# Performance work log

Measured on AMD Instinct MI355X. Metric: run time of the kernel, lower is better.

Reference implementation:

```python
import jax, jax.numpy as jnp
import numpy as np

N_NODES = 100000


def _gcn_conv(x, W, b, src, dst, n):
    """torch_geometric GCNConv: add self-loops, sym-normalize, x@W, scatter-add."""
    x = x @ W                                   # [n, out]
    loop = jnp.arange(n, dtype=src.dtype)
    src_f = jnp.concatenate([src, loop])        # [E+n]
    dst_f = jnp.concatenate([dst, loop])
    deg = jax.ops.segment_sum(jnp.ones_like(dst_f, dtype=x.dtype), dst_f,
                              num_segments=n)   # in-degree incl. self-loop
    dinv = jnp.where(deg > 0, jax.lax.rsqrt(deg), 0.0)
    norm = dinv[src_f] * dinv[dst_f]            # [E+n]
    msg = x[src_f] * norm[:, None]              # [E+n, out]
    out = jax.ops.segment_sum(msg, dst_f, num_segments=n)
    return out + b


def setup_inputs() -> dict:
    key = jax.random.key(0)
    k1, k2, k3, k4 = jax.random.split(key, 4)
    ninp = 64
    E = 1600000
    edge_index = jax.random.randint(k1, (2, E), 0, N_NODES, dtype=jnp.int64)
    emb = jax.random.normal(k2, (N_NODES, ninp), dtype=jnp.float32) * (1.0 / np.sqrt(ninp))
    W1 = jax.random.normal(k3, (ninp, 2 * ninp), dtype=jnp.float32) * (1.0 / np.sqrt(ninp))
    b1 = jnp.zeros((2 * ninp,), dtype=jnp.float32)
    W2 = jax.random.normal(k4, (2 * ninp, ninp), dtype=jnp.float32) * (1.0 / np.sqrt(2 * ninp))
    b2 = jnp.zeros((ninp,), dtype=jnp.float32)
    return {"edge_index": edge_index, "emb": emb, "W1": W1, "b1": b1, "W2": W2, "b2": b2}


def reference(edge_index, emb, W1, b1, W2, b2):
    src, dst = edge_index[0], edge_index[1]
    h = jax.nn.relu(_gcn_conv(emb, W1, b1, src, dst, N_NODES))
    # dropout: eval mode (identity)
    out = _gcn_conv(h, W2, b2, src, dst, N_NODES)
    return out
```

## Files before the change

kernel.cpp:

```cpp
#include <hip/hip_runtime.h>
#include <cstdint>
#include <cstddef>

#define N_NODES_C 100000
#define NF 64
#define BW 512
#define NB 196
#define CHUNK 8192
#define SORT_CAP 9216

static inline size_t align256(size_t x) { return (x + 255) & ~size_t(255); }

typedef __attribute__((ext_vector_type(8))) short bf16x8;
typedef __attribute__((ext_vector_type(4))) float f32x4;

__device__ inline float bf2f(unsigned short u) { return __uint_as_float(((unsigned)u) << 16); }
__device__ inline unsigned short f2bf(float x) {
    unsigned u = __float_as_uint(x);
    return (unsigned short)((u + 0x7fffu + ((u >> 16) & 1u)) >> 16);
}

__global__ __launch_bounds__(1024) void bucket_count(const int* __restrict__ dst, int E,
                                                     int* __restrict__ counts) {
    __shared__ int hist[NB];
    int t = threadIdx.x;
    for (int i = t; i < NB; i += 1024) hist[i] = 0;
    __syncthreads();
    int e0 = blockIdx.x * CHUNK;
    int e1 = min(e0 + CHUNK, E);
    for (int e = e0 + t; e < e1; e += 1024) atomicAdd(&hist[dst[e] >> 9], 1);
    __syncthreads();
    for (int i = t; i < NB; i += 1024)
        if (hist[i]) atomicAdd(&counts[i], hist[i]);
}

__global__ void scan196(const int* __restrict__ counts, int* __restrict__ base196,
                        int* __restrict__ bucket_cursor, int* __restrict__ row_start, int n) {
    int lane = threadIdx.x;
    int base = 0;
    for (int c = 0; c < NB; c += 64) {
        int idx = c + lane;
        int v = (idx < NB) ? counts[idx] : 0;
        int x = v;
        #pragma unroll
        for (int d = 1; d < 64; d <<= 1) {
            int y = __shfl_up(x, d, 64);
            if (lane >= d) x += y;
        }
        if (idx < NB) { base196[idx] = base + x - v; bucket_cursor[idx] = base + x - v; }
        base += __shfl(x, 63, 64);
    }
    if (lane == 0) { base196[NB] = base; row_start[n] = base; }
}

__global__ __launch_bounds__(1024) void bin_kernel(const int* __restrict__ src,
                                                   const int* __restrict__ dst, int E,
                                                   int* __restrict__ bucket_cursor,
                                                   int* __restrict__ packed) {
    __shared__ int hist[NB];
    __shared__ int lbase[NB];
    __shared__ int lcur[NB];
    __shared__ int gbase[NB];
    __shared__ int stage[CHUNK];
    __shared__ unsigned char bid[CHUNK];
    int t = threadIdx.x;
    int e0 = blockIdx.x * CHUNK;
    int e1 = min(e0 + CHUNK, E);
    for (int i = t; i < NB; i += 1024) hist[i] = 0;
    __syncthreads();
    for (int e = e0 + t; e < e1; e += 1024) atomicAdd(&hist[dst[e] >> 9], 1);
    __syncthreads();
    if (t < 64) {
        int base = 0;
        for (int c = 0; c < NB; c += 64) {
            int idx = c + t;
            int v = (idx < NB) ? hist[idx] : 0;
            int x = v;
            #pragma unroll
            for (int d = 1; d < 64; d <<= 1) {
                int y = __shfl_up(x, d, 64);
                if (t >= d) x += y;
            }
            if (idx < NB) { lbase[idx] = base + x - v; lcur[idx] = base + x - v; }
            base += __shfl(x, 63, 64);
        }
    }
    __syncthreads();
    if (t < NB) gbase[t] = atomicAdd(&bucket_cursor[t], hist[t]);
    for (int e = e0 + t; e < e1; e += 1024) {
        int d = dst[e];
        int b = d >> 9;
        int p = atomicAdd(&lcur[b], 1);
        stage[p] = (src[e] << 9) | (d & (BW - 1));
        bid[p] = (unsigned char)b;
    }
    __syncthreads();
    int cnt = e1 - e0;
    for (int i = t; i < cnt; i += 1024) {
        int b = bid[i];
        packed[gbase[b] + (i - lbase[b])] = stage[i];
    }
}

__global__ __launch_bounds__(512) void bucket_sort_deg(const int* __restrict__ base196,
                                                       const int* __restrict__ packed,
                                                       int* __restrict__ sorted_src,
                                                       int* __restrict__ row_start,
                                                       float* __restrict__ dinv, int n) {
    __shared__ int hist[BW];
    __shared__ int cur[BW];
    __shared__ int wsum[8];
    __shared__ int sorted[SORT_CAP];
    int b = blockIdx.x;
    int node0 = b * BW;
    int nn = min(BW, n - node0);
    int base = base196[b];
    int end = base196[b + 1];
    int cnt = end - base;
    int t = threadIdx.x;
    hist[t] = 0;
    __syncthreads();
    for (int i = t; i < cnt; i += 512) atomicAdd(&hist[packed[base + i] & (BW - 1)], 1);
    __syncthreads();
    int v = hist[t];
    int lane = t & 63, w = t >> 6;
    int x = v;
    #pragma unroll
    for (int d = 1; d < 64; d <<= 1) {
        int y = __shfl_up(x, d, 64);
        if (lane >= d) x += y;
    }
    if (lane == 63) wsum[w] = x;
    __syncthreads();
    int woff = 0;
    for (int i = 0; i < w; ++i) woff += wsum[i];
    int excl = woff + x - v;
    cur[t] = excl;
    if (t < nn) {
        row_start[node0 + t] = base + excl;
        dinv[node0 + t] = rsqrtf((float)(v + 1));
    }
    __syncthreads();
    for (int i = t; i < cnt; i += 512) {
        int pk = packed[base + i];
        int p = atomicAdd(&cur[pk & (BW - 1)], 1);
        sorted[p] = pk >> 9;
    }
    __syncthreads();
    for (int i = t; i < cnt; i += 512) sorted_src[base + i] = sorted[i];
}

__global__ __launch_bounds__(256) void prep_w(const float* __restrict__ W1,
                                              const float* __restrict__ W2,
                                              unsigned short* __restrict__ W1f,
                                              unsigned short* __restrict__ W2f) {
    int idx = blockIdx.x * 256 + threadIdx.x;
    int lane = (idx >> 3) & 63;
    int j = idx & 7;
    int kk = (lane >> 4) * 8 + j;
    int cb = lane & 15;
    if (idx < 8192) {
        int frag = idx >> 9;
        int ct = frag >> 1, ks = frag & 1;
        W1f[idx] = f2bf(W1[(ks * 32 + kk) * 128 + ct * 16 + cb]);
    } else {
        int i2 = idx - 8192;
        int frag = i2 >> 9;
        int ct = frag >> 2, ks = frag & 3;
        W2f[i2] = f2bf(W2[(ks * 32 + kk) * 64 + ct * 16 + cb]);
    }
}

__global__ __launch_bounds__(256) void scale_emb(const float* __restrict__ emb,
                                                 const float* __restrict__ dinv,
                                                 unsigned short* __restrict__ Xs, int nq) {
    int q = blockIdx.x * 256 + threadIdx.x;
    if (q >= nq) return;
    int node = q >> 4;
    float d = dinv[node];
    float4 v = ((const float4*)emb)[q];
    ushort4 u;
    u.x = f2bf(v.x * d); u.y = f2bf(v.y * d);
    u.z = f2bf(v.z * d); u.w = f2bf(v.w * d);
    *(ushort4*)&Xs[(size_t)q * 4] = u;
}

template<int OUTBF>
__global__ __launch_bounds__(256) void agg_bf16(const unsigned short* __restrict__ Xs,
                                                const float* __restrict__ dinv,
                                                const int* __restrict__ row_start,
                                                const int* __restrict__ sorted_src,
                                                const float* __restrict__ bias,
                                                void* __restrict__ outp, int n) {
    int lane = threadIdx.x & 63;
    int wid = threadIdx.x >> 6;
    int wave = blockIdx.x * (blockDim.x >> 6) + wid;
    int nwaves = gridDim.x * (blockDim.x >> 6);
    int e = lane >> 4;
    int c = lane & 15;
    const int ZOFF = -64;
    for (int i = wave; i < n; i += nwaves) {
        int s0 = row_start[i], s1 = row_start[i + 1];
        float di = dinv[i];
        ushort4 uself = *(const ushort4*)&Xs[(size_t)i * NF + 4 * c];
        float a0 = 0.f, a1 = 0.f, a2 = 0.f, a3 = 0.f;
        float g0 = 0.f, g1 = 0.f, g2 = 0.f, g3 = 0.f;
        for (int j = s0; j < s1; j += 16) {
            int b0 = j + 4 * e;
            int sj0 = b0, sj1 = b0 + 1, sj2 = b0 + 2, sj3 = b0 + 3;
            int i0 = sorted_src[min(sj0, s1 - 1)];
            int i1 = sorted_src[min(sj1, s1 - 1)];
            int i2 = sorted_src[min(sj2, s1 - 1)];
            int i3 = sorted_src[min(sj3, s1 - 1)];
            int o0 = (sj0 < s1) ? (i0 << 6) : ZOFF;
            int o1 = (sj1 < s1) ? (i1 << 6) : ZOFF;
            int o2 = (sj2 < s1) ? (i2 << 6) : ZOFF;
            int o3 = (sj3 < s1) ? (i3 << 6) : ZOFF;
            ushort4 u0 = *(const ushort4*)(Xs + o0 + 4 * c);
            ushort4 u1 = *(const ushort4*)(Xs + o1 + 4 * c);
            ushort4 u2 = *(const ushort4*)(Xs + o2 + 4 * c);
            ushort4 u3 = *(const ushort4*)(Xs + o3 + 4 * c);
            a0 += bf2f(u0.x); a1 += bf2f(u0.y); a2 += bf2f(u0.z); a3 += bf2f(u0.w);
            g0 += bf2f(u1.x); g1 += bf2f(u1.y); g2 += bf2f(u1.z); g3 += bf2f(u1.w);
            a0 += bf2f(u2.x); a1 += bf2f(u2.y); a2 += bf2f(u2.z); a3 += bf2f(u2.w);
            g0 += bf2f(u3.x); g1 += bf2f(u3.y); g2 += bf2f(u3.z); g3 += bf2f(u3.w);
        }
        a0 += g0; a1 += g1; a2 += g2; a3 += g3;
        a0 += __shfl_xor(a0, 16, 64); a1 += __shfl_xor(a1, 16, 64);
        a2 += __shfl_xor(a2, 16, 64); a3 += __shfl_xor(a3, 16, 64);
        a0 += __shfl_xor(a0, 32, 64); a1 += __shfl_xor(a1, 32, 64);
        a2 += __shfl_xor(a2, 32, 64); a3 += __shfl_xor(a3, 32, 64);
        if (e == 0) {
            a0 = di * (a0 + bf2f(uself.x));
            a1 = di * (a1 + bf2f(uself.y));
            a2 = di * (a2 + bf2f(uself.z));
            a3 = di * (a3 + bf2f(uself.w));
            if (bias) {
                float4 bb = *(const float4*)&bias[4 * c];
                a0 += bb.x; a1 += bb.y; a2 += bb.z; a3 += bb.w;
            }
            if constexpr (OUTBF) {
                unsigned short* out = (unsigned short*)outp;
                ushort4 o;
                o.x = f2bf(a0); o.y = f2bf(a1); o.z = f2bf(a2); o.w = f2bf(a3);
                *(ushort4*)&out[(size_t)i * NF + 4 * c] = o;
            } else {
                float* out = (float*)outp;
                float4 o; o.x = a0; o.y = a1; o.z = a2; o.w = a3;
                *(float4*)&out[(size_t)i * NF + 4 * c] = o;
            }
        }
    }
}

__global__ __launch_bounds__(256) void gemm_mfma(const unsigned short* __restrict__ Abf,
                                                 const unsigned short* __restrict__ W1f,
                                                 const float* __restrict__ b1,
                                                 const unsigned short* __restrict__ W2f,
                                                 const float* __restrict__ dinv,
                                                 unsigned short* __restrict__ Tbf, int n) {
    __shared__ unsigned short h_all[4][16 * 136];
    const int t = threadIdx.x;
    const int wid = t >> 6, lane = t & 63;
    const int m = lane & 15, kg = lane >> 4;
    const int wrow = blockIdx.x * 64 + wid * 16;
    unsigned short* h_lds = h_all[wid];

    int arow = wrow + m; if (arow >= n) arow = n - 1;
    bf16x8 a0 = *(const bf16x8*)&Abf[(size_t)arow * 64 + kg * 8];
    bf16x8 a1 = *(const bf16x8*)&Abf[(size_t)arow * 64 + 32 + kg * 8];

    #pragma unroll
    for (int ct = 0; ct < 8; ++ct) {
        f32x4 acc = {0.f, 0.f, 0.f, 0.f};
        bf16x8 w0 = *(const bf16x8*)&W1f[(ct * 2 + 0) * 512 + lane * 8];
        bf16x8 w1 = *(const bf16x8*)&W1f[(ct * 2 + 1) * 512 + lane * 8];
        acc = __builtin_amdgcn_mfma_f32_16x16x32_bf16(a0, w0, acc, 0, 0, 0);
        acc = __builtin_amdgcn_mfma_f32_16x16x32_bf16(a1, w1, acc, 0, 0, 0);
        float bb = b1[ct * 16 + m];
        #pragma unroll
        for (int r = 0; r < 4; ++r) {
            float v = fmaxf(acc[r] + bb, 0.f);
            h_lds[(kg * 4 + r) * 136 + ct * 16 + m] = f2bf(v);
        }
    }

    bf16x8 hf[4];
    #pragma unroll
    for (int ks = 0; ks < 4; ++ks)
        hf[ks] = *(const bf16x8*)&h_lds[m * 136 + ks * 32 + kg * 8];

    float dv[4];
    #pragma unroll
    for (int r = 0; r < 4; ++r) {
        int row = wrow + kg * 4 + r;
        dv[r] = (row < n) ? dinv[row] : 0.f;
    }
    #pragma unroll
    for (int ct = 0; ct < 4; ++ct) {
        f32x4 acc = {0.f, 0.f, 0.f, 0.f};
        #pragma unroll
        for (int ks = 0; ks < 4; ++ks) {
            bf16x8 w = *(const bf16x8*)&W2f[(ct * 4 + ks) * 512 + lane * 8];
            acc = __builtin_amdgcn_mfma_f32_16x16x32_bf16(hf[ks], w, acc, 0, 0, 0);
        }
        #pragma unroll
        for (int r = 0; r < 4; ++r) {
            int row = wrow + kg * 4 + r;
            if (row < n) Tbf[(size_t)row * 64 + ct * 16 + m] = f2bf(acc[r] * dv[r]);
        }
    }
}

extern "C" void kernel_launch(void* const* d_in, const int* in_sizes, int n_in,
                              void* d_out, int out_size, void* d_ws, size_t ws_size,
                              hipStream_t stream) {
    const int* edge = (const int*)d_in[0];
    const float* emb = (const float*)d_in[1];
    const float* W1  = (const float*)d_in[2];
    const float* b1  = (const float*)d_in[3];
    const float* W2  = (const float*)d_in[4];
    const float* b2  = (const float*)d_in[5];
    int E = in_sizes[0] / 2;
    const int* src = edge;
    const int* dst = edge + E;
    int n = N_NODES_C;

    char* p = (char*)d_ws;
    int*   row_start  = (int*)p;   p += align256((size_t)(n + 1) * 4);
    float* dinv       = (float*)p; p += align256((size_t)n * 4);
    int*   bcounts    = (int*)p;   p += align256(256 * 4);
    int*   base196    = (int*)p;   p += align256(256 * 4);
    int*   bucket_cur = (int*)p;   p += align256(256 * 4);
    unsigned short* W1f = (unsigned short*)p; p += align256(8192 * 2);
    unsigned short* W2f = (unsigned short*)p; p += align256(8192 * 2);
    int*   sorted_src = (int*)p;   p += align256((size_t)E * 4);
    char*  zpadA      = p;         p += 256;
    unsigned short* Abf = (unsigned short*)p; p += align256((size_t)n * NF * 2);
    char*  zpadX      = p;         p += 256;
    unsigned short* Xs  = (unsigned short*)p; p += align256((size_t)n * NF * 2);
    int* packed = (int*)Abf;

    prep_w<<<64, 256, 0, stream>>>(W1, W2, W1f, W2f);
    hipMemsetAsync(bcounts, 0, NB * 4, stream);
    hipMemsetAsync(zpadA, 0, 256, stream);
    hipMemsetAsync(zpadX, 0, 256, stream);
    int nbin = (E + CHUNK - 1) / CHUNK;
    bucket_count<<<nbin, 1024, 0, stream>>>(dst, E, bcounts);
    scan196<<<1, 64, 0, stream>>>(bcounts, base196, bucket_cur, row_start, n);
    bin_kernel<<<nbin, 1024, 0, stream>>>(src, dst, E, bucket_cur, packed);
    bucket_sort_deg<<<NB, 512, 0, stream>>>(base196, packed, sorted_src, row_start, dinv, n);

    int nq = n * 16;
    scale_emb<<<(nq + 255) / 256, 256, 0, stream>>>(emb, dinv, Xs, nq);
    agg_bf16<1><<<4096, 256, 0, stream>>>(Xs, dinv, row_start, sorted_src, nullptr, Abf, n);
    gemm_mfma<<<(n + 63) / 64, 256, 0, stream>>>(Abf, W1f, b1, W2f, dinv, Xs, n);
    agg_bf16<0><<<4096, 256, 0, stream>>>(Xs, dinv, row_start, sorted_src, b2, d_out, n);
}
```

Before: 150.6 us.

## Replace global atomic bucket cursors with per-chunk histogram scan for deterministic binning

Each chunk's bucket histogram is now stored to global memory, and a column-wise scan gives every chunk a fixed offset within each bucket. The binning kernel then reads these offsets instead of rescanning dst to rebuild the histogram and taking global atomic cursors. The three memsets are folded into the small scan kernel, which cuts launch count. In exchange it adds one scan kernel launch and extra histogram and partial-offset buffers in the workspace.

```diff
diff --git a/kernel.cpp b/kernel.cpp
--- a/kernel.cpp
+++ b/kernel.cpp
@@ -20,8 +20,8 @@
     return (unsigned short)((u + 0x7fffu + ((u >> 16) & 1u)) >> 16);
 }
 
-__global__ __launch_bounds__(1024) void bucket_count(const int* __restrict__ dst, int E,
-                                                     int* __restrict__ counts) {
+__global__ __launch_bounds__(1024) void count_hist(const int* __restrict__ dst, int E,
+                                                   int* __restrict__ chunk_hist) {
     __shared__ int hist[NB];
     int t = threadIdx.x;
     for (int i = t; i < NB; i += 1024) hist[i] = 0;
@@ -30,45 +30,71 @@
     int e1 = min(e0 + CHUNK, E);
     for (int e = e0 + t; e < e1; e += 1024) atomicAdd(&hist[dst[e] >> 9], 1);
     __syncthreads();
-    for (int i = t; i < NB; i += 1024)
-        if (hist[i]) atomicAdd(&counts[i], hist[i]);
-}
-
-__global__ void scan196(const int* __restrict__ counts, int* __restrict__ base196,
-                        int* __restrict__ bucket_cursor, int* __restrict__ row_start, int n) {
+    for (int i = t; i < NB; i += 1024) chunk_hist[blockIdx.x * NB + i] = hist[i];
+}
+
+__global__ void scan_cols(const int* __restrict__ chunk_hist, int nbin,
+                          int* __restrict__ gpart, int* __restrict__ colsum) {
+    int b = blockIdx.x;
     int lane = threadIdx.x;
+    int base = 0;
+    for (int c0 = 0; c0 < nbin; c0 += 64) {
+        int c = c0 + lane;
+        int v = (c < nbin) ? chunk_hist[c * NB + b] : 0;
+        int x = v;
+        #pragma unroll
+        for (int d = 1; d < 64; d <<= 1) {
+            int y = __shfl_up(x, d, 64);
+            if (lane >= d) x += y;
+        }
+        if (c < nbin) gpart[c * NB + b] = base + x - v;
+        base += __shfl(x, 63, 64);
+    }
+    if (lane == 0) colsum[b] = base;
+}
+
+__global__ void scan196b(const int* __restrict__ colsum, int* __restrict__ base196,
+                         int* __restrict__ row_start, int n,
+                         int* __restrict__ zpadA, int* __restrict__ zpadX) {
+    int lane = threadIdx.x;
+    zpadA[lane] = 0;
+    zpadX[lane] = 0;
     int base = 0;
     for (int c = 0; c < NB; c += 64) {
         int idx = c + lane;
-        int v = (idx < NB) ? counts[idx] : 0;
+        int v = (idx < NB) ? colsum[idx] : 0;
         int x = v;
         #pragma unroll
         for (int d = 1; d < 64; d <<= 1) {
             int y = __shfl_up(x, d, 64);
             if (lane >= d) x += y;
         }
-        if (idx < NB) { base196[idx] = base + x - v; bucket_cursor[idx] = base + x - v; }
+        if (idx < NB) base196[idx] = base + x - v;
         base += __shfl(x, 63, 64);
     }
     if (lane == 0) { base196[NB] = base; row_start[n] = base; }
 }
 
-__global__ __launch_bounds__(1024) void bin_kernel(const int* __restrict__ src,
-                                                   const int* __restrict__ dst, int E,
-                                                   int* __restrict__ bucket_cursor,
-                                                   int* __restrict__ packed) {
+__global__ __launch_bounds__(1024) void bin_kernel2(const int* __restrict__ src,
+                                                    const int* __restrict__ dst, int E,
+                                                    const int* __restrict__ chunk_hist,
+                                                    const int* __restrict__ gpart,
+                                                    const int* __restrict__ base196,
+                                                    int* __restrict__ packed) {
     __shared__ int hist[NB];
     __shared__ int lbase[NB];
     __shared__ int lcur[NB];
-    __shared__ int gbase[NB];
+    __shared__ int dbase[NB];
     __shared__ int stage[CHUNK];
     __shared__ unsigned char bid[CHUNK];
     int t = threadIdx.x;
-    int e0 = blockIdx.x * CHUNK;
+    int ch = blockIdx.x;
+    int e0 = ch * CHUNK;
     int e1 = min(e0 + CHUNK, E);
-    for (int i = t; i < NB; i += 1024) hist[i] = 0;
-    __syncthreads();
-    for (int e = e0 + t; e < e1; e += 1024) atomicAdd(&hist[dst[e] >> 9], 1);
+    for (int i = t; i < NB; i += 1024) {
+        hist[i] = chunk_hist[ch * NB + i];
+        dbase[i] = base196[i] + gpart[ch * NB + i];
+    }
     __syncthreads();
     if (t < 64) {
         int base = 0;
@@ -86,7 +112,6 @@
         }
     }
     __syncthreads();
-    if (t < NB) gbase[t] = atomicAdd(&bucket_cursor[t], hist[t]);
     for (int e = e0 + t; e < e1; e += 1024) {
         int d = dst[e];
         int b = d >> 9;
@@ -98,7 +123,7 @@
     int cnt = e1 - e0;
     for (int i = t; i < cnt; i += 1024) {
         int b = bid[i];
-        packed[gbase[b] + (i - lbase[b])] = stage[i];
+        packed[dbase[b] + (i - lbase[b])] = stage[i];
     }
 }
 
@@ -325,30 +350,29 @@
     const int* src = edge;
     const int* dst = edge + E;
     int n = N_NODES_C;
+    int nbin = (E + CHUNK - 1) / CHUNK;
 
     char* p = (char*)d_ws;
     int*   row_start  = (int*)p;   p += align256((size_t)(n + 1) * 4);
     float* dinv       = (float*)p; p += align256((size_t)n * 4);
-    int*   bcounts    = (int*)p;   p += align256(256 * 4);
     int*   base196    = (int*)p;   p += align256(256 * 4);
-    int*   bucket_cur = (int*)p;   p += align256(256 * 4);
+    int*   colsum     = (int*)p;   p += align256(256 * 4);
+    int*   chunk_hist = (int*)p;   p += align256((size_t)nbin * NB * 4);
+    int*   gpart      = (int*)p;   p += align256((size_t)nbin * NB * 4);
     unsigned short* W1f = (unsigned short*)p; p += align256(8192 * 2);
     unsigned short* W2f = (unsigned short*)p; p += align256(8192 * 2);
     int*   sorted_src = (int*)p;   p += align256((size_t)E * 4);
-    char*  zpadA      = p;         p += 256;
+    int*   zpadA      = (int*)p;   p += 256;
     unsigned short* Abf = (unsigned short*)p; p += align256((size_t)n * NF * 2);
-    char*  zpadX      = p;         p += 256;
+    int*   zpadX      = (int*)p;   p += 256;
     unsigned short* Xs  = (unsigned short*)p; p += align256((size_t)n * NF * 2);
     int* packed = (int*)Abf;
 
     prep_w<<<64, 256, 0, stream>>>(W1, W2, W1f, W2f);
-    hipMemsetAsync(bcounts, 0, NB * 4, stream);
-    hipMemsetAsync(zpadA, 0, 256, stream);
-    hipMemsetAsync(zpadX, 0, 256, stream);
-    int nbin = (E + CHUNK - 1) / CHUNK;
-    bucket_count<<<nbin, 1024, 0, stream>>>(dst, E, bcounts);
-    scan196<<<1, 64, 0, stream>>>(bcounts, base196, bucket_cur, row_start, n);
-    bin_kernel<<<nbin, 1024, 0, stream>>>(src, dst, E, bucket_cur, packed);
+    count_hist<<<nbin, 1024, 0, stream>>>(dst, E, chunk_hist);
+    scan_cols<<<NB, 64, 0, stream>>>(chunk_hist, nbin, gpart, colsum);
+    scan196b<<<1, 64, 0, stream>>>(colsum, base196, row_start, n, zpadA, zpadX);
+    bin_kernel2<<<nbin, 1024, 0, stream>>>(src, dst, E, chunk_hist, gpart, base196, packed);
     bucket_sort_deg<<<NB, 512, 0, stream>>>(base196, packed, sorted_src, row_start, dinv, n);
 
     int nq = n * 16;
```

Result: faster. 140.6 us (-6.7%).
